# Kernel tuning notes

Hardware: AMD Instinct MI355X
Metric: run time of the kernel (lower is better)

The kernel has to match this reference:

```python
import jax, jax.numpy as jnp
import numpy as np

B, S, C = 8, 2048, 512

def setup_inputs() -> dict:
    key = jax.random.key(0)
    ks = jax.random.split(key, 7)
    s = 1.0 / np.sqrt(C)
    return {
        "x": jax.random.normal(ks[0], (B, S, C), dtype=jnp.float32),
        "Wq": jax.random.uniform(ks[1], (C, C), jnp.float32, -s, s),
        "bq": jax.random.uniform(ks[2], (C,), jnp.float32, -s, s),
        "Wk": jax.random.uniform(ks[3], (C, C), jnp.float32, -s, s),
        "bk": jax.random.uniform(ks[4], (C,), jnp.float32, -s, s),
        "Wv": jax.random.uniform(ks[5], (C, C), jnp.float32, -s, s),
        "bv": jax.random.uniform(ks[6], (C,), jnp.float32, -s, s),
    }

def reference(x, Wq, bq, Wk, bk, Wv, bv):
    # Linear projections (torch Linear: x @ W.T + b)
    q = jnp.einsum('bsc,dc->bsd', x, Wq) + bq
    k = jnp.einsum('bsc,dc->bsd', x, Wk) + bk
    v = jnp.einsum('bsc,dc->bsd', x, Wv) + bv
    # NOTE: original code computes dk but never scales by 1/sqrt(dk)
    scores = jnp.einsum('bqd,bkd->bqk', q, k)          # [B,S,S]
    attn = jax.nn.softmax(scores, axis=-1)
    out = jnp.einsum('bqk,bkd->bqd', attn, v)
    return out + x
```

## Files before the change

kernel.cpp:

```cpp
#include <hip/hip_runtime.h>
#include <hip/hip_bf16.h>


typedef __bf16 bf16_t;
typedef bf16_t bf16x8 __attribute__((ext_vector_type(8)));
typedef float floatx4 __attribute__((ext_vector_type(4)));

#define MFMA16(a, b, c) __builtin_amdgcn_mfma_f32_16x16x32_bf16((a), (b), (c), 0, 0, 0)
#define FLASH_LDS 75264

__device__ __forceinline__ void gload16(const void* g, void* l) {
    __builtin_amdgcn_global_load_lds((const __attribute__((address_space(1))) void*)g,
                                     (__attribute__((address_space(3))) void*)l, 16, 0, 0);
}

__device__ __forceinline__ float wave16_sum(float v) {
    v += __shfl_xor(v, 1);
    v += __shfl_xor(v, 2);
    v += __shfl_xor(v, 4);
    v += __shfl_xor(v, 8);
    return v;
}

__global__ void convert_in(const float* __restrict__ X,
                           const float* __restrict__ Wq, const float* __restrict__ Wk,
                           const float* __restrict__ Wv, const float* __restrict__ bq,
                           const float* __restrict__ bk, const float* __restrict__ bv,
                           bf16_t* __restrict__ Xb, bf16_t* __restrict__ Wb,
                           float* __restrict__ biasc) {
    int bid = blockIdx.x, tid = threadIdx.x;
    if (bid < 4096) {
        size_t e0 = ((size_t)bid * 256 + tid) * 8;
        float4 f0 = *(const float4*)(X + e0);
        float4 f1 = *(const float4*)(X + e0 + 4);
        bf16x8 o;
        o[0] = (bf16_t)f0.x; o[1] = (bf16_t)f0.y; o[2] = (bf16_t)f0.z; o[3] = (bf16_t)f0.w;
        o[4] = (bf16_t)f1.x; o[5] = (bf16_t)f1.y; o[6] = (bf16_t)f1.z; o[7] = (bf16_t)f1.w;
        *(bf16x8*)(Xb + e0) = o;
    } else {
        int idx = (bid - 4096) * 256 + tid;
        int e0 = idx * 4;
        int row = e0 >> 9, c = e0 & 511;
        const float* src;
        if (row < 512)       src = Wq + row * 512;
        else if (row < 1024) src = Wk + (row - 512) * 512;
        else                 src = Wv + (row - 1024) * 512;
        float4 v = *(const float4*)(src + c);
        Wb[e0 + 0] = (bf16_t)v.x;
        Wb[e0 + 1] = (bf16_t)v.y;
        Wb[e0 + 2] = (bf16_t)v.z;
        Wb[e0 + 3] = (bf16_t)v.w;
        if (idx < 1536) {
            float b;
            if (idx < 512)       b = bq[idx];
            else if (idx < 1024) b = bk[idx - 512];
            else                 b = bv[idx - 1024];
            biasc[idx] = b;
        }
    }
}

__global__ __launch_bounds__(256, 2)
void qkv_gemm(const bf16_t* __restrict__ Xb, const bf16_t* __restrict__ Wb,
              const float* __restrict__ biasc, bf16_t* __restrict__ Q,
              bf16_t* __restrict__ K, bf16_t* __restrict__ Vt) {
    __shared__ int4 smem4[2560];
    char* As = (char*)smem4;
    char* Bs = (char*)smem4 + 16384;
    char* Vtile = (char*)smem4;

    const int tid = threadIdx.x;
    const int l = tid & 63, w = tid >> 6;
    const int lane16 = l & 15, lq = l >> 4;
    const int klo = lane16 & 7;
    const int m0 = (blockIdx.x & 127) << 7;
    const int n0 = (blockIdx.x >> 7) << 7;
    const int wm = (w >> 1) << 6, wn = (w & 1) << 6;
    const int srow = l >> 3;
    const int sc8 = (l & 7) ^ srow;

    floatx4 acc[4][4];
#pragma unroll
    for (int a = 0; a < 4; ++a)
#pragma unroll
        for (int bb = 0; bb < 4; ++bb) acc[a][bb] = (floatx4){0.f, 0.f, 0.f, 0.f};

    for (int it = 0; it < 8; ++it) {
        __syncthreads();
#pragma unroll
        for (int j = 0; j < 4; ++j) {
            int seg = j * 4 + w;
            int row = seg * 8 + srow;
            gload16(Xb + (size_t)(m0 + row) * 512 + it * 64 + sc8 * 8, As + seg * 1024);
            gload16(Wb + (size_t)(n0 + row) * 512 + it * 64 + sc8 * 8, Bs + seg * 1024);
        }
        __syncthreads();
#pragma unroll
        for (int kst = 0; kst < 2; ++kst) {
            bf16x8 afr[4], bfr[4];
#pragma unroll
            for (int mt = 0; mt < 4; ++mt)
                afr[mt] = *(const bf16x8*)(As + (wm + mt * 16 + lane16) * 128 +
                                           ((kst * 4 + lq) ^ klo) * 16);
#pragma unroll
            for (int nt = 0; nt < 4; ++nt)
                bfr[nt] = *(const bf16x8*)(Bs + (wn + nt * 16 + lane16) * 128 +
                                           ((kst * 4 + lq) ^ klo) * 16);
#pragma unroll
            for (int mt = 0; mt < 4; ++mt)
#pragma unroll
                for (int nt = 0; nt < 4; ++nt)
                    acc[mt][nt] = MFMA16(afr[mt], bfr[nt], acc[mt][nt]);
        }
    }

    float bias_v[4];
#pragma unroll
    for (int nt = 0; nt < 4; ++nt) bias_v[nt] = biasc[n0 + wn + nt * 16 + lane16];

    if (n0 < 1024) {
        bf16_t* Dst = (n0 < 512) ? Q : K;
        const int coff = (n0 < 512 ? n0 : n0 - 512) + wn;
#pragma unroll
        for (int mt = 0; mt < 4; ++mt)
#pragma unroll
            for (int nt = 0; nt < 4; ++nt)
#pragma unroll
                for (int i = 0; i < 4; ++i) {
                    int rowM = m0 + wm + mt * 16 + lq * 4 + i;
                    Dst[(size_t)rowM * 512 + coff + nt * 16 + lane16] =
                        (bf16_t)(acc[mt][nt][i] + bias_v[nt]);
                }
    } else {
        __syncthreads();
#pragma unroll
        for (int mt = 0; mt < 4; ++mt)
#pragma unroll
            for (int nt = 0; nt < 4; ++nt)
#pragma unroll
                for (int i = 0; i < 4; ++i) {
                    int dl = wn + nt * 16 + lane16;
                    int sl = wm + mt * 16 + lq * 4 + i;
                    *(bf16_t*)(Vtile + dl * 264 + sl * 2) =
                        (bf16_t)(acc[mt][nt][i] + bias_v[nt]);
                }
        __syncthreads();
        const int bb = m0 >> 11, s0 = m0 & 2047, dbase = n0 - 1024;
#pragma unroll
        for (int j = 0; j < 8; ++j) {
            int slot = j * 256 + tid;
            int dd = slot >> 4, c = slot & 15;
            *(int4*)(Vt + (size_t)(bb * 512 + dbase + dd) * 2048 + s0 + c * 8) =
                *(const int4*)(Vtile + dd * 264 + c * 16);
        }
    }
}

__global__ __launch_bounds__(512, 2)
void flash_attn_v6(const bf16_t* __restrict__ Q, const bf16_t* __restrict__ K,
                   const bf16_t* __restrict__ Vt, const float* __restrict__ X,
                   float* __restrict__ Out) {
    extern __shared__ char smem[];
    char* Ks = smem;
    char* Ps = smem + 65536;
    float* lpart = (float*)(smem + 74752);

    const int tid = threadIdx.x;
    const int l = tid & 63, w = tid >> 6;
    const int lane16 = l & 15, lq = l >> 4;
    const int qg = w >> 1, h = w & 1;
    const int dbase = w << 6;
    const int b = blockIdx.x & 7;
    const int q0 = (blockIdx.x >> 3) << 6;

    const bf16_t* Kbase = K + (size_t)b * 2048 * 512;
    const bf16_t* Vbase = Vt + (size_t)b * 512 * 2048;

#pragma unroll
    for (int j = 0; j < 8; ++j) {
        int seg = j * 8 + w;
        int c = (l & ~7) | ((l & 7) ^ (seg & 7));
        gload16(Kbase + (size_t)seg * 512 + c * 8, Ks + seg * 1024);
    }

    bf16x8 qf[16];
    const bf16_t* Qrow = Q + (size_t)(b * 2048 + q0 + qg * 16 + lane16) * 512 + lq * 8;
#pragma unroll
    for (int kst = 0; kst < 16; ++kst) qf[kst] = *(const bf16x8*)(Qrow + kst * 32);

    floatx4 o[16];
#pragma unroll
    for (int t = 0; t < 16; ++t) o[t] = (floatx4){0.f, 0.f, 0.f, 0.f};
    float lsum[4] = {0.f, 0.f, 0.f, 0.f};
    const float L2E = 1.4426950408889634f;

    __syncthreads();

    for (int kt = 0; kt < 32; ++kt) {
        floatx4 scA[2], scB[2];
#pragma unroll
        for (int g = 0; g < 2; ++g) {
            scA[g] = (floatx4){0.f, 0.f, 0.f, 0.f};
            scB[g] = (floatx4){0.f, 0.f, 0.f, 0.f};
        }
#pragma unroll
        for (int kst = 0; kst < 16; kst += 2) {
#pragma unroll
            for (int g = 0; g < 2; ++g) {
                int key = h * 32 + g * 16 + lane16;
                int i0 = kst * 4 + lq;
                int i1 = i0 + 4;
                int p0 = (i0 & ~7) | ((i0 & 7) ^ (key & 7));
                int p1 = (i1 & ~7) | ((i1 & 7) ^ (key & 7));
                bf16x8 kb0 = *(const bf16x8*)(Ks + key * 1024 + p0 * 16);
                bf16x8 kb1 = *(const bf16x8*)(Ks + key * 1024 + p1 * 16);
                scA[g] = MFMA16(qf[kst], kb0, scA[g]);
                scB[g] = MFMA16(qf[kst + 1], kb1, scB[g]);
            }
        }

        bf16x8 vb[8];
        {
            const bf16_t* Vsrc = Vbase + kt * 64;
#pragma unroll
            for (int dg = 0; dg < 4; ++dg) {
                int d = dbase + dg * 16 + lane16;
#pragma unroll
                for (int kk = 0; kk < 2; ++kk)
                    vb[dg * 2 + kk] =
                        *(const bf16x8*)(Vsrc + (size_t)d * 2048 + kk * 32 + lq * 8);
            }
        }

#pragma unroll
        for (int g = 0; g < 2; ++g) {
            int keyc = h * 32 + g * 16 + lane16;
#pragma unroll
            for (int i = 0; i < 4; ++i) {
                float p = __builtin_exp2f((scA[g][i] + scB[g][i]) * L2E);
                lsum[i] += p;
                *(bf16_t*)(Ps + (qg * 16 + lq * 4 + i) * 144 + keyc * 2) = (bf16_t)p;
            }
        }
        __syncthreads();

        if (kt < 31) {
            const bf16_t* Ksrc = Kbase + (size_t)(kt + 1) * 64 * 512;
#pragma unroll
            for (int j = 0; j < 8; ++j) {
                int seg = j * 8 + w;
                int c = (l & ~7) | ((l & 7) ^ (seg & 7));
                gload16(Ksrc + (size_t)seg * 512 + c * 8, Ks + seg * 1024);
            }
        }
#pragma unroll
        for (int kk = 0; kk < 2; ++kk) {
            bf16x8 pa[4];
#pragma unroll
            for (int qgi = 0; qgi < 4; ++qgi)
                pa[qgi] = *(const bf16x8*)(Ps + (qgi * 16 + lane16) * 144 + kk * 64 + lq * 16);
#pragma unroll
            for (int dg = 0; dg < 4; ++dg)
#pragma unroll
                for (int qgi = 0; qgi < 4; ++qgi)
                    o[qgi * 4 + dg] = MFMA16(pa[qgi], vb[dg * 2 + kk], o[qgi * 4 + dg]);
        }
        __syncthreads();
    }

#pragma unroll
    for (int i = 0; i < 4; ++i) {
        float s = wave16_sum(lsum[i]);
        if (lane16 == 0) lpart[(qg * 16 + lq * 4 + i) * 2 + h] = s;
    }
    __syncthreads();

#pragma unroll
    for (int qgi = 0; qgi < 4; ++qgi) {
        float rinv[4];
#pragma unroll
        for (int i = 0; i < 4; ++i) {
            int row = qgi * 16 + lq * 4 + i;
            rinv[i] = 1.0f / (lpart[row * 2] + lpart[row * 2 + 1]);
        }
#pragma unroll
        for (int dg = 0; dg < 4; ++dg) {
            int d = dbase + dg * 16 + lane16;
#pragma unroll
            for (int i = 0; i < 4; ++i) {
                int row = q0 + qgi * 16 + lq * 4 + i;
                size_t g = (size_t)(b * 2048 + row) * 512 + d;
                Out[g] = o[qgi * 4 + dg][i] * rinv[i] + X[g];
            }
        }
    }
}

extern "C" void kernel_launch(void* const* d_in, const int* in_sizes, int n_in,
                              void* d_out, int out_size, void* d_ws, size_t ws_size,
                              hipStream_t stream) {
    const float* x  = (const float*)d_in[0];
    const float* Wq = (const float*)d_in[1];
    const float* bq = (const float*)d_in[2];
    const float* Wk = (const float*)d_in[3];
    const float* bk = (const float*)d_in[4];
    const float* Wv = (const float*)d_in[5];
    const float* bv = (const float*)d_in[6];
    float* out = (float*)d_out;
    char* ws = (char*)d_ws;

    bf16_t* Wb    = (bf16_t*)(ws);
    float*  biasc = (float*)(ws + 1572864);
    bf16_t* Xb    = (bf16_t*)(ws + 1579008);
    bf16_t* Qb    = (bf16_t*)(ws + 18356224);
    bf16_t* Kb    = (bf16_t*)(ws + 35133440);
    bf16_t* Vt    = (bf16_t*)(ws + 51910656);

    convert_in<<<4864, 256, 0, stream>>>(x, Wq, Wk, Wv, bq, bk, bv, Xb, Wb, biasc);
    qkv_gemm<<<1536, 256, 0, stream>>>(Xb, Wb, biasc, Qb, Kb, Vt);

    hipFuncSetAttribute(reinterpret_cast<const void*>(flash_attn_v6),
                        hipFuncAttributeMaxDynamicSharedMemorySize, FLASH_LDS);
    flash_attn_v6<<<256, 512, FLASH_LDS, stream>>>(Qb, Kb, Vt, x, out);
}
```

Baseline: 240.5 us.

## Double-buffer K and V tiles in LDS with async prefetch in flash attention

Restructures the attention loop to use 32-key tiles and stages both K and V into double-buffered LDS via async global-to-LDS loads, prefetching the next tile while computing the current one. V is no longer loaded from global memory straight into registers inside the loop, and V uses a swizzled LDS layout. This is meant to hide global load latency. In exchange it raises LDS use per block, which limits blocks per CU, doubles the number of iterations and barriers, and serializes the score MFMA chain.

After: 221.6 us. -7.9%, faster.

```diff
diff --git a/kernel.cpp b/kernel.cpp
--- a/kernel.cpp
+++ b/kernel.cpp
@@ -7,7 +7,7 @@
 typedef float floatx4 __attribute__((ext_vector_type(4)));
 
 #define MFMA16(a, b, c) __builtin_amdgcn_mfma_f32_16x16x32_bf16((a), (b), (c), 0, 0, 0)
-#define FLASH_LDS 75264
+#define FLASH_LDS 136704
 
 __device__ __forceinline__ void gload16(const void* g, void* l) {
     __builtin_amdgcn_global_load_lds((const __attribute__((address_space(1))) void*)g,
@@ -157,13 +157,12 @@
 }
 
 __global__ __launch_bounds__(512, 2)
-void flash_attn_v6(const bf16_t* __restrict__ Q, const bf16_t* __restrict__ K,
+void flash_attn_v7(const bf16_t* __restrict__ Q, const bf16_t* __restrict__ K,
                    const bf16_t* __restrict__ Vt, const float* __restrict__ X,
                    float* __restrict__ Out) {
     extern __shared__ char smem[];
-    char* Ks = smem;
-    char* Ps = smem + 65536;
-    float* lpart = (float*)(smem + 74752);
+    char* Ps = smem + 131072;
+    float* lpart = (float*)(smem + 136192);
 
     const int tid = threadIdx.x;
     const int l = tid & 63, w = tid >> 6;
@@ -176,12 +175,29 @@
     const bf16_t* Kbase = K + (size_t)b * 2048 * 512;
     const bf16_t* Vbase = Vt + (size_t)b * 512 * 2048;
 
-#pragma unroll
-    for (int j = 0; j < 8; ++j) {
-        int seg = j * 8 + w;
-        int c = (l & ~7) | ((l & 7) ^ (seg & 7));
-        gload16(Kbase + (size_t)seg * 512 + c * 8, Ks + seg * 1024);
-    }
+    const int dl_v = ((l >> 3) << 1) | ((l & 7) >> 2);
+    const int vc   = (l & 3) ^ ((l >> 3) & 3);
+
+    auto stageK = [&](int kt, char* Kb) {
+#pragma unroll
+        for (int j = 0; j < 4; ++j) {
+            int seg = j * 8 + w;
+            int c = (l & ~7) | ((l & 7) ^ (seg & 7));
+            gload16(Kbase + ((size_t)kt * 32 + seg) * 512 + c * 8, Kb + seg * 1024);
+        }
+    };
+    auto stageV = [&](int kt, char* Vb) {
+        const bf16_t* Vsrc = Vbase + kt * 32;
+#pragma unroll
+        for (int j = 0; j < 4; ++j) {
+            int seg = j * 8 + w;
+            int d = seg * 16 + dl_v;
+            gload16(Vsrc + (size_t)d * 2048 + vc * 8, Vb + seg * 1024);
+        }
+    };
+
+    stageK(0, smem);
+    stageV(0, smem + 65536);
 
     bf16x8 qf[16];
     const bf16_t* Qrow = Q + (size_t)(b * 2048 + q0 + qg * 16 + lane16) * 512 + lq * 8;
@@ -193,78 +209,55 @@
     for (int t = 0; t < 16; ++t) o[t] = (floatx4){0.f, 0.f, 0.f, 0.f};
     float lsum[4] = {0.f, 0.f, 0.f, 0.f};
     const float L2E = 1.4426950408889634f;
+    const int key = h * 16 + lane16;
 
     __syncthreads();
 
-    for (int kt = 0; kt < 32; ++kt) {
-        floatx4 scA[2], scB[2];
-#pragma unroll
-        for (int g = 0; g < 2; ++g) {
-            scA[g] = (floatx4){0.f, 0.f, 0.f, 0.f};
-            scB[g] = (floatx4){0.f, 0.f, 0.f, 0.f};
-        }
-#pragma unroll
-        for (int kst = 0; kst < 16; kst += 2) {
-#pragma unroll
-            for (int g = 0; g < 2; ++g) {
-                int key = h * 32 + g * 16 + lane16;
-                int i0 = kst * 4 + lq;
-                int i1 = i0 + 4;
-                int p0 = (i0 & ~7) | ((i0 & 7) ^ (key & 7));
-                int p1 = (i1 & ~7) | ((i1 & 7) ^ (key & 7));
-                bf16x8 kb0 = *(const bf16x8*)(Ks + key * 1024 + p0 * 16);
-                bf16x8 kb1 = *(const bf16x8*)(Ks + key * 1024 + p1 * 16);
-                scA[g] = MFMA16(qf[kst], kb0, scA[g]);
-                scB[g] = MFMA16(qf[kst + 1], kb1, scB[g]);
-            }
-        }
-
-        bf16x8 vb[8];
-        {
-            const bf16_t* Vsrc = Vbase + kt * 64;
-#pragma unroll
-            for (int dg = 0; dg < 4; ++dg) {
-                int d = dbase + dg * 16 + lane16;
-#pragma unroll
-                for (int kk = 0; kk < 2; ++kk)
-                    vb[dg * 2 + kk] =
-                        *(const bf16x8*)(Vsrc + (size_t)d * 2048 + kk * 32 + lq * 8);
-            }
-        }
-
-#pragma unroll
-        for (int g = 0; g < 2; ++g) {
-            int keyc = h * 32 + g * 16 + lane16;
-#pragma unroll
-            for (int i = 0; i < 4; ++i) {
-                float p = __builtin_exp2f((scA[g][i] + scB[g][i]) * L2E);
-                lsum[i] += p;
-                *(bf16_t*)(Ps + (qg * 16 + lq * 4 + i) * 144 + keyc * 2) = (bf16_t)p;
-            }
-        }
-        __syncthreads();
-
-        if (kt < 31) {
-            const bf16_t* Ksrc = Kbase + (size_t)(kt + 1) * 64 * 512;
-#pragma unroll
-            for (int j = 0; j < 8; ++j) {
-                int seg = j * 8 + w;
-                int c = (l & ~7) | ((l & 7) ^ (seg & 7));
-                gload16(Ksrc + (size_t)seg * 512 + c * 8, Ks + seg * 1024);
-            }
-        }
-#pragma unroll
-        for (int kk = 0; kk < 2; ++kk) {
-            bf16x8 pa[4];
+    for (int kt = 0; kt < 64; ++kt) {
+        char* Kcur = smem + (kt & 1) * 32768;
+        char* Vcur = smem + 65536 + (kt & 1) * 32768;
+
+        if (kt < 63) {
+            stageK(kt + 1, smem + ((kt + 1) & 1) * 32768);
+            stageV(kt + 1, smem + 65536 + ((kt + 1) & 1) * 32768);
+        }
+
+        floatx4 sc = (floatx4){0.f, 0.f, 0.f, 0.f};
+#pragma unroll
+        for (int kst = 0; kst < 16; ++kst) {
+            int i0 = kst * 4 + lq;
+            int p0 = (i0 & ~7) | ((i0 & 7) ^ (key & 7));
+            bf16x8 kb = *(const bf16x8*)(Kcur + key * 1024 + p0 * 16);
+            sc = MFMA16(qf[kst], kb, sc);
+        }
+
+#pragma unroll
+        for (int i = 0; i < 4; ++i) {
+            int row = qg * 16 + lq * 4 + i;
+            float p = __builtin_exp2f(sc[i] * L2E);
+            lsum[i] += p;
+            *(bf16_t*)(Ps + row * 80 + key * 2) = (bf16_t)p;
+        }
+
+        asm volatile("s_waitcnt lgkmcnt(0)\n\ts_barrier" ::: "memory");
+        __builtin_amdgcn_sched_barrier(0);
+
+        bf16x8 pa[4], vb[4];
+#pragma unroll
+        for (int qgi = 0; qgi < 4; ++qgi)
+            pa[qgi] = *(const bf16x8*)(Ps + (qgi * 16 + lane16) * 80 + lq * 16);
+#pragma unroll
+        for (int dg = 0; dg < 4; ++dg) {
+            int d = dbase + dg * 16 + lane16;
+            int slot = (d & 1) * 4 + (lq ^ ((d >> 1) & 3));
+            vb[dg] = *(const bf16x8*)(Vcur + (d >> 1) * 128 + slot * 16);
+        }
+#pragma unroll
+        for (int dg = 0; dg < 4; ++dg)
 #pragma unroll
             for (int qgi = 0; qgi < 4; ++qgi)
-                pa[qgi] = *(const bf16x8*)(Ps + (qgi * 16 + lane16) * 144 + kk * 64 + lq * 16);
-#pragma unroll
-            for (int dg = 0; dg < 4; ++dg)
-#pragma unroll
-                for (int qgi = 0; qgi < 4; ++qgi)
-                    o[qgi * 4 + dg] = MFMA16(pa[qgi], vb[dg * 2 + kk], o[qgi * 4 + dg]);
-        }
+                o[qgi * 4 + dg] = MFMA16(pa[qgi], vb[dg], o[qgi * 4 + dg]);
+
         __syncthreads();
     }
 
@@ -319,7 +312,7 @@
     convert_in<<<4864, 256, 0, stream>>>(x, Wq, Wk, Wv, bq, bk, bv, Xb, Wb, biasc);
     qkv_gemm<<<1536, 256, 0, stream>>>(Xb, Wb, biasc, Qb, Kb, Vt);
 
-    hipFuncSetAttribute(reinterpret_cast<const void*>(flash_attn_v6),
+    hipFuncSetAttribute(reinterpret_cast<const void*>(flash_attn_v7),
                         hipFuncAttributeMaxDynamicSharedMemorySize, FLASH_LDS);
-    flash_attn_v6<<<256, 512, FLASH_LDS, stream>>>(Qb, Kb, Vt, x, out);
-}
+    flash_attn_v7<<<256, 512, FLASH_LDS, stream>>>(Qb, Kb, Vt, x, out);
+}
```
